# Kernel optimization log

Measured on AMD Instinct MI355X. Metric: run time of the kernel, lower is better.

## Reference

```python
import jax, jax.numpy as jnp
import numpy as np

N, D, H, M = 8192, 64, 4096, 2
EPS = 1e-12  # F.normalize eps


def setup_inputs() -> dict:
    key = jax.random.key(0)
    k0, k1, k2, k3, k4 = jax.random.split(key, 5)
    # spins in {-1, +1}
    x = (2 * jax.random.randint(k0, (N, D), 0, 2) - 1).astype(jnp.float32)
    W1 = jax.random.normal(k1, (D, H), jnp.float32) * 0.05
    b1 = jax.random.normal(k2, (H,), jnp.float32) * 0.05
    W2 = jax.random.normal(k3, (H, M), jnp.float32) * 0.05
    b2 = jax.random.normal(k4, (M,), jnp.float32) * 0.05
    return {"x": x, "W1": W1, "b1": b1, "W2": W2, "b2": b2}


def reference(x, W1, b1, W2, b2):
    # Per step d: mask off sites >= d, run MLP, L2-normalize the 2 amplitudes,
    # select psi_pos/psi_neg by the spin at site d, accumulate product.
    n, d_sites = x.shape
    site_idx = jnp.arange(d_sites)

    def step(wav, d):
        mask = (site_idx < d).astype(x.dtype)          # [D], sites 0..d-1 visible
        h = jnp.tanh((x * mask) @ W1 + b1)             # [N, H]
        out = jnp.tanh(h @ W2 + b2)                    # [N, 2]
        norm = jnp.maximum(
            jnp.sqrt(jnp.sum(out * out, axis=1, keepdims=True)), EPS)
        out = out / norm                               # F.normalize(out, 2)
        sel = jnp.where(x[:, d] > 0, out[:, 0], out[:, 1])
        return wav * sel, None

    wav0 = jnp.ones((n,), x.dtype)
    wav, _ = jax.lax.scan(step, wav0, jnp.arange(d_sites))
    return wav
```

## Files before the change

kernel.cpp:

```cpp
#include <hip/hip_runtime.h>
#include <math.h>

#define NS 8192
#define DS 64
#define HD 4096
#define C2L 2.8853900817779268f

__device__ __forceinline__ float fast_tanh(float x) {
    float t = __builtin_amdgcn_exp2f(x * C2L);
    float r = __builtin_amdgcn_rcpf(t + 1.0f);
    return __builtin_fmaf(-2.0f, r, 1.0f);
}

__global__ __launch_bounds__(256) void qnade_prep_E(
    const float* __restrict__ W1, float* __restrict__ Ep, float* __restrict__ Em)
{
    int i = blockIdx.x * 256 + threadIdx.x;
    float w = W1[i] * C2L;
    Ep[i] = __builtin_amdgcn_exp2f(w);
    Em[i] = __builtin_amdgcn_exp2f(-w);
}

__global__ __launch_bounds__(256) void qnade_prep_S(
    const float* __restrict__ W2, const float* __restrict__ b2, float* __restrict__ C01)
{
    __shared__ float p0[4], p1[4];
    int tid = threadIdx.x;
    float s0 = 0.0f, s1 = 0.0f;
    for (int h = tid; h < HD; h += 256) {
        float2 w = ((const float2*)W2)[h];
        s0 += w.x; s1 += w.y;
    }
    #pragma unroll
    for (int m = 1; m < 64; m <<= 1) {
        s0 += __shfl_xor(s0, m, 64);
        s1 += __shfl_xor(s1, m, 64);
    }
    if ((tid & 63) == 0) { p0[tid >> 6] = s0; p1[tid >> 6] = s1; }
    __syncthreads();
    if (tid == 0) {
        C01[0] = p0[0] + p0[1] + p0[2] + p0[3] + b2[0];
        C01[1] = p1[0] + p1[1] + p1[2] + p1[3] + b2[1];
    }
}

__global__ __launch_bounds__(256) void qnade_main(
    const float* __restrict__ x, const float* __restrict__ b1,
    const float* __restrict__ W2, const float* __restrict__ Ep,
    const float* __restrict__ Em, const float* __restrict__ C01,
    float* __restrict__ out)
{
    __shared__ float parts[DS * 64];

    const int tid  = threadIdx.x;
    const int lane = tid & 63;
    const int wv   = tid >> 6;
    const int n    = blockIdx.x;
    const int hbase = wv * 1024 + lane * 4;

    float w20[16], w21[16];
    #pragma unroll
    for (int q = 0; q < 4; ++q) {
        const float4* p = (const float4*)(W2 + 2 * (hbase + q * 256));
        float4 A = p[0], B = p[1];
        w20[q*4+0] = A.x; w21[q*4+0] = A.y;
        w20[q*4+1] = A.z; w21[q*4+1] = A.w;
        w20[q*4+2] = B.x; w21[q*4+2] = B.y;
        w20[q*4+3] = B.z; w21[q*4+3] = B.w;
    }

    float t[16];
    #pragma unroll
    for (int q = 0; q < 4; ++q) {
        float4 b = *(const float4*)(b1 + hbase + q * 256);
        t[q*4+0] = __builtin_amdgcn_exp2f(b.x * C2L);
        t[q*4+1] = __builtin_amdgcn_exp2f(b.y * C2L);
        t[q*4+2] = __builtin_amdgcn_exp2f(b.z * C2L);
        t[q*4+3] = __builtin_amdgcn_exp2f(b.w * C2L);
    }

    const float xv = x[n * DS + lane];

    for (int d = 0; d < DS; ++d) {
        float xd = __shfl(xv, d, 64);
        const float* E = (__builtin_amdgcn_readfirstlane(xd > 0.0f ? 1 : 0) ? Ep : Em)
                         + d * HD + hbase;
        float acc0 = 0.0f, acc1 = 0.0f;
        #pragma unroll
        for (int q = 0; q < 4; ++q) {
            float4 e = *(const float4*)(E + q * 256);
            #pragma unroll
            for (int c = 0; c < 4; ++c) {
                const int j = q * 4 + c;
                float tv = t[j];
                float r  = __builtin_amdgcn_rcpf(1.0f + tv);
                acc0 = __builtin_fmaf(r, w20[j], acc0);
                acc1 = __builtin_fmaf(r, w21[j], acc1);
                float ec = (c == 0) ? e.x : (c == 1) ? e.y : (c == 2) ? e.z : e.w;
                t[j] = tv * ec;
            }
        }
        acc0 += __shfl_xor(acc0, 8, 64);
        acc0 += __shfl_xor(acc0, 16, 64);
        acc0 += __shfl_xor(acc0, 32, 64);
        acc1 += __shfl_xor(acc1, 8, 64);
        acc1 += __shfl_xor(acc1, 16, 64);
        acc1 += __shfl_xor(acc1, 32, 64);
        if (lane < 8) {
            parts[d * 64 + wv * 16 + lane]     = acc0;
            parts[d * 64 + wv * 16 + 8 + lane] = acc1;
        }
    }

    __syncthreads();

    if (tid < DS) {
        const int d = tid;
        const float* p = parts + d * 64;
        float s0 = 0.0f, s1 = 0.0f;
        #pragma unroll
        for (int w = 0; w < 4; ++w) {
            #pragma unroll
            for (int i = 0; i < 8; ++i) {
                s0 += p[w * 16 + i];
                s1 += p[w * 16 + 8 + i];
            }
        }
        float dot0 = __builtin_fmaf(-2.0f, s0, C01[0]);
        float dot1 = __builtin_fmaf(-2.0f, s1, C01[1]);
        float o0 = fast_tanh(dot0);
        float o1 = fast_tanh(dot1);
        float nrm = sqrtf(__builtin_fmaf(o0, o0, o1 * o1));
        nrm = fmaxf(nrm, 1e-12f);
        float sel = (x[n * DS + d] > 0.0f) ? o0 : o1;
        float v = sel * __builtin_amdgcn_rcpf(nrm);
        v *= __shfl_xor(v, 1, 64);
        v *= __shfl_xor(v, 2, 64);
        v *= __shfl_xor(v, 4, 64);
        v *= __shfl_xor(v, 8, 64);
        v *= __shfl_xor(v, 16, 64);
        v *= __shfl_xor(v, 32, 64);
        if (tid == 0) out[n] = v;
    }
}

__global__ __launch_bounds__(256) void qnade_fallback(
    const float* __restrict__ x, const float* __restrict__ W1,
    const float* __restrict__ b1, const float* __restrict__ W2,
    const float* __restrict__ b2, float* __restrict__ out)
{
    __shared__ __align__(16) float w20s[HD];
    __shared__ __align__(16) float w21s[HD];
    const int tid = threadIdx.x;
    for (int i = tid; i < HD; i += 256) {
        float2 w = ((const float2*)W2)[i];
        w20s[i] = w.x;
        w21s[i] = w.y;
    }
    const int lane = tid & 63;
    const int wv   = tid >> 6;
    const int n    = (blockIdx.x << 2) + wv;
    const float b20 = b2[0];
    const float b21 = b2[1];
    const float xv = x[n * DS + lane];
    float4 a[16];
    const float4* b1v = (const float4*)b1;
    #pragma unroll
    for (int q = 0; q < 16; ++q) a[q] = b1v[q * 64 + lane];
    __syncthreads();
    const float4* w20v = (const float4*)w20s;
    const float4* w21v = (const float4*)w21s;
    float wav = 1.0f;
    for (int d = 0; d < DS; ++d) {
        const float xd = __shfl(xv, d, 64);
        const float4* w1v = (const float4*)(W1 + d * HD);
        float dot0 = 0.0f, dot1 = 0.0f;
        #pragma unroll
        for (int q = 0; q < 16; ++q) {
            float4 w1 = w1v[q * 64 + lane];
            float4 av = a[q];
            float h0 = fast_tanh(av.x);
            float h1 = fast_tanh(av.y);
            float h2 = fast_tanh(av.z);
            float h3 = fast_tanh(av.w);
            float4 c0 = w20v[q * 64 + lane];
            float4 c1 = w21v[q * 64 + lane];
            dot0 = fmaf(h0, c0.x, dot0); dot0 = fmaf(h1, c0.y, dot0);
            dot0 = fmaf(h2, c0.z, dot0); dot0 = fmaf(h3, c0.w, dot0);
            dot1 = fmaf(h0, c1.x, dot1); dot1 = fmaf(h1, c1.y, dot1);
            dot1 = fmaf(h2, c1.z, dot1); dot1 = fmaf(h3, c1.w, dot1);
            av.x = fmaf(xd, w1.x, av.x); av.y = fmaf(xd, w1.y, av.y);
            av.z = fmaf(xd, w1.z, av.z); av.w = fmaf(xd, w1.w, av.w);
            a[q] = av;
        }
        #pragma unroll
        for (int m = 1; m < 64; m <<= 1) {
            dot0 += __shfl_xor(dot0, m, 64);
            dot1 += __shfl_xor(dot1, m, 64);
        }
        float o0 = fast_tanh(dot0 + b20);
        float o1 = fast_tanh(dot1 + b21);
        float nrm = sqrtf(fmaf(o0, o0, o1 * o1));
        nrm = fmaxf(nrm, 1e-12f);
        float sel = (xd > 0.0f) ? o0 : o1;
        wav *= sel / nrm;
    }
    out[n] = wav;
}

extern "C" void kernel_launch(void* const* d_in, const int* in_sizes, int n_in,
                              void* d_out, int out_size, void* d_ws, size_t ws_size,
                              hipStream_t stream) {
    const float* x  = (const float*)d_in[0];
    const float* W1 = (const float*)d_in[1];
    const float* b1 = (const float*)d_in[2];
    const float* W2 = (const float*)d_in[3];
    const float* b2 = (const float*)d_in[4];
    float* out = (float*)d_out;

    const size_t need = (size_t)(2 * DS * HD + 2) * sizeof(float);
    if (ws_size >= need) {
        float* Ep  = (float*)d_ws;
        float* Em  = Ep + DS * HD;
        float* C01 = Em + DS * HD;
        hipLaunchKernelGGL(qnade_prep_E, dim3(DS * HD / 256), dim3(256), 0, stream, W1, Ep, Em);
        hipLaunchKernelGGL(qnade_prep_S, dim3(1), dim3(256), 0, stream, W2, b2, C01);
        hipLaunchKernelGGL(qnade_main, dim3(NS), dim3(256), 0, stream, x, b1, W2, Ep, Em, C01, out);
    } else {
        hipLaunchKernelGGL(qnade_fallback, dim3(NS / 4), dim3(256), 0, stream, x, W1, b1, W2, b2, out);
    }
}
```

Before: 447.1 us.

## Batch reciprocals via prefix products and use packed fp32 math in main loop

```diff
diff --git a/kernel.cpp b/kernel.cpp
--- a/kernel.cpp
+++ b/kernel.cpp
@@ -5,6 +5,18 @@
 #define DS 64
 #define HD 4096
 #define C2L 2.8853900817779268f
+
+typedef float v2f __attribute__((ext_vector_type(2)));
+
+__device__ __forceinline__ v2f pk_add(v2f a, v2f b) {
+    v2f d; asm("v_pk_add_f32 %0, %1, %2" : "=v"(d) : "v"(a), "v"(b)); return d;
+}
+__device__ __forceinline__ v2f pk_mul(v2f a, v2f b) {
+    v2f d; asm("v_pk_mul_f32 %0, %1, %2" : "=v"(d) : "v"(a), "v"(b)); return d;
+}
+__device__ __forceinline__ v2f pk_fma(v2f a, v2f b, v2f c) {
+    v2f d; asm("v_pk_fma_f32 %0, %1, %2, %3" : "=v"(d) : "v"(a), "v"(b), "v"(c)); return d;
+}
 
 __device__ __forceinline__ float fast_tanh(float x) {
     float t = __builtin_amdgcn_exp2f(x * C2L);
@@ -58,57 +70,78 @@
     const int n    = blockIdx.x;
     const int hbase = wv * 1024 + lane * 4;
 
-    float w20[16], w21[16];
+    v2f w20[8], w21[8];
     #pragma unroll
     for (int q = 0; q < 4; ++q) {
         const float4* p = (const float4*)(W2 + 2 * (hbase + q * 256));
         float4 A = p[0], B = p[1];
-        w20[q*4+0] = A.x; w21[q*4+0] = A.y;
-        w20[q*4+1] = A.z; w21[q*4+1] = A.w;
-        w20[q*4+2] = B.x; w21[q*4+2] = B.y;
-        w20[q*4+3] = B.z; w21[q*4+3] = B.w;
-    }
-
-    float t[16];
+        w20[2*q]   = (v2f){A.x, A.z};  w21[2*q]   = (v2f){A.y, A.w};
+        w20[2*q+1] = (v2f){B.x, B.z};  w21[2*q+1] = (v2f){B.y, B.w};
+    }
+
+    v2f t2[8];
     #pragma unroll
     for (int q = 0; q < 4; ++q) {
         float4 b = *(const float4*)(b1 + hbase + q * 256);
-        t[q*4+0] = __builtin_amdgcn_exp2f(b.x * C2L);
-        t[q*4+1] = __builtin_amdgcn_exp2f(b.y * C2L);
-        t[q*4+2] = __builtin_amdgcn_exp2f(b.z * C2L);
-        t[q*4+3] = __builtin_amdgcn_exp2f(b.w * C2L);
+        t2[2*q]   = (v2f){__builtin_amdgcn_exp2f(b.x * C2L), __builtin_amdgcn_exp2f(b.y * C2L)};
+        t2[2*q+1] = (v2f){__builtin_amdgcn_exp2f(b.z * C2L), __builtin_amdgcn_exp2f(b.w * C2L)};
     }
 
     const float xv = x[n * DS + lane];
-
+    const unsigned long long msk = __ballot(xv > 0.0f);
+    const v2f one = (v2f){1.0f, 1.0f};
+
+    #pragma unroll 1
     for (int d = 0; d < DS; ++d) {
-        float xd = __shfl(xv, d, 64);
-        const float* E = (__builtin_amdgcn_readfirstlane(xd > 0.0f ? 1 : 0) ? Ep : Em)
-                         + d * HD + hbase;
-        float acc0 = 0.0f, acc1 = 0.0f;
-        #pragma unroll
-        for (int q = 0; q < 4; ++q) {
-            float4 e = *(const float4*)(E + q * 256);
-            #pragma unroll
-            for (int c = 0; c < 4; ++c) {
-                const int j = q * 4 + c;
-                float tv = t[j];
-                float r  = __builtin_amdgcn_rcpf(1.0f + tv);
-                acc0 = __builtin_fmaf(r, w20[j], acc0);
-                acc1 = __builtin_fmaf(r, w21[j], acc1);
-                float ec = (c == 0) ? e.x : (c == 1) ? e.y : (c == 2) ? e.z : e.w;
-                t[j] = tv * ec;
-            }
-        }
-        acc0 += __shfl_xor(acc0, 8, 64);
-        acc0 += __shfl_xor(acc0, 16, 64);
-        acc0 += __shfl_xor(acc0, 32, 64);
-        acc1 += __shfl_xor(acc1, 8, 64);
-        acc1 += __shfl_xor(acc1, 16, 64);
-        acc1 += __shfl_xor(acc1, 32, 64);
+        const float* E = (((msk >> d) & 1ull) ? Ep : Em) + d * HD + hbase;
+        float4 e0 = *(const float4*)(E);
+        float4 e1 = *(const float4*)(E + 256);
+        float4 e2 = *(const float4*)(E + 512);
+        float4 e3 = *(const float4*)(E + 768);
+
+        v2f u2[8], p2[8];
+        #pragma unroll
+        for (int j = 0; j < 8; ++j) u2[j] = pk_add(t2[j], one);
+        p2[0] = u2[0];
+        #pragma unroll
+        for (int j = 1; j < 8; ++j) p2[j] = pk_mul(p2[j - 1], u2[j]);
+        float P = p2[7].x * p2[7].y;
+        float R = __builtin_amdgcn_rcpf(P);
+        v2f RR = (v2f){R * p2[7].y, R * p2[7].x};
+        v2f r2[8];
+        #pragma unroll
+        for (int j = 7; j >= 1; --j) {
+            r2[j] = pk_mul(RR, p2[j - 1]);
+            RR    = pk_mul(RR, u2[j]);
+        }
+        r2[0] = RR;
+
+        v2f acc0 = (v2f){0.0f, 0.0f}, acc1 = (v2f){0.0f, 0.0f};
+        #pragma unroll
+        for (int j = 0; j < 8; ++j) {
+            acc0 = pk_fma(r2[j], w20[j], acc0);
+            acc1 = pk_fma(r2[j], w21[j], acc1);
+        }
+        t2[0] = pk_mul(t2[0], (v2f){e0.x, e0.y});
+        t2[1] = pk_mul(t2[1], (v2f){e0.z, e0.w});
+        t2[2] = pk_mul(t2[2], (v2f){e1.x, e1.y});
+        t2[3] = pk_mul(t2[3], (v2f){e1.z, e1.w});
+        t2[4] = pk_mul(t2[4], (v2f){e2.x, e2.y});
+        t2[5] = pk_mul(t2[5], (v2f){e2.z, e2.w});
+        t2[6] = pk_mul(t2[6], (v2f){e3.x, e3.y});
+        t2[7] = pk_mul(t2[7], (v2f){e3.z, e3.w});
+
+        float a0 = acc0.x + acc0.y;
+        float a1 = acc1.x + acc1.y;
+        a0 += __shfl_xor(a0, 8, 64);
+        a0 += __shfl_xor(a0, 16, 64);
+        a0 += __shfl_xor(a0, 32, 64);
+        a1 += __shfl_xor(a1, 8, 64);
+        a1 += __shfl_xor(a1, 16, 64);
+        a1 += __shfl_xor(a1, 32, 64);
         if (lane < 8) {
-            parts[d * 64 + wv * 16 + lane]     = acc0;
-            parts[d * 64 + wv * 16 + 8 + lane] = acc1;
+            parts[d * 64 + wv * 16 + lane]     = a0;
+            parts[d * 64 + wv * 16 + 8 + lane] = a1;
         }
     }
 
```

New measurement: 468.1 us. +4.7%, slower.
